# Kernel tuning notes

Measured on AMD Instinct MI355X. Metric: run time of the kernel, lower is better.

Reference implementation:

```python
import jax, jax.numpy as jnp
import numpy as np

# Grid / modeling constants (match init_kwargs)
NX, NY = 512, 512
NT = 400
ORDER = 8
NE = ORDER // 2          # halo width
H = 10.0                 # grid spacing (m)
DT = 0.001               # time step (s)
DIMX = NX + ORDER
DIMY = NY + ORDER
# 8th-order second-derivative FD coefficients
C0, C1, C2, C3, C4 = -205.0 / 72.0, 8.0 / 5.0, -1.0 / 5.0, 8.0 / 315.0, -1.0 / 560.0
_COEF = (C1, C2, C3, C4)


def setup_inputs() -> dict:
    key = jax.random.key(0)
    k1, k2 = jax.random.split(key)
    # realistic acoustic velocity model, 1500-2500 m/s
    vel = 1500.0 + 1000.0 * jax.random.uniform(k1, (NX, NY), dtype=jnp.float32)
    w = jax.random.normal(k2, (NT,), dtype=jnp.float32)  # source wavelet
    return {"vel": vel, "w": w, "sx": 256, "sy": 4, "ry": 4}


def _laplacian(u):
    # order-8 cross stencil in x and y (grid is (dimy, dimx), x fast)
    l = 2.0 * C0 * u
    for k, c in zip((1, 2, 3, 4), _COEF):
        l = l + c * (jnp.roll(u, k, 0) + jnp.roll(u, -k, 0)
                     + jnp.roll(u, k, 1) + jnp.roll(u, -k, 1))
    return l


def _forward(vel, w, sx, sy, ry):
    # vel: (nx, ny) y-fast -> vpad: (dimy, dimx) x-fast, replication padded
    vpad = jnp.pad(vel.T, NE, mode="edge")
    scale = (vpad * DT) ** 2 / (H * H)          # (v*dt/h)^2 per cell
    mask = jnp.zeros((DIMY, DIMX), vel.dtype).at[NE:NE + NY, NE:NE + NX].set(1.0)
    iy, ix = sy + NE, sx + NE
    src_amp = (vpad[iy, ix] * DT) ** 2           # dt^2 * v^2 at source

    def step(carry, wt):
        u1, u2 = carry
        lap = _laplacian(u2)
        u3 = (2.0 * u2 - u1 + scale * lap) * mask  # zero Dirichlet halo
        u3 = u3.at[iy, ix].add(wt * src_amp)       # source injection
        rec = u3[ry + NE, NE:NE + NX]              # record x-line at depth ry
        return (u2, u3), rec

    u0 = jnp.zeros((DIMY, DIMX), vel.dtype)
    _, frd = jax.lax.scan(jax.checkpoint(step), (u0, u0), w)
    return frd  # (nt, nx)


def reference(vel, w, sx, sy, ry):
    return _forward(vel, w, sx, sy, ry)
```

## Files before the change

### kernel.cpp

```cpp
#include <hip/hip_runtime.h>

typedef float f32x4 __attribute__((ext_vector_type(4)));

#define NXg   512
#define NYg   512
#define NTt   400
#define DIMg  520
#define DTc   0.001f
#define Hc    10.0f

#define TILE   80
#define TSTR   84
#define NQROW  20
#define NQUADS (TILE*NQROW)

#define C0f (-205.0f/72.0f)
#define C1f (8.0f/5.0f)
#define C2f (-1.0f/5.0f)
#define C3f (8.0f/315.0f)
#define C4f (-1.0f/560.0f)

__global__ void time2d_init(const float* __restrict__ vel,
                            const float* __restrict__ w,
                            const int* __restrict__ sxp,
                            const int* __restrict__ syp,
                            const int* __restrict__ ryp,
                            float* __restrict__ scale,
                            float* __restrict__ fields,
                            float* __restrict__ params) {
    int idx = blockIdx.x * blockDim.x + threadIdx.x;
    if (idx < DIMg * DIMg) {
        int y = idx / DIMg;
        int x = idx - y * DIMg;
        float s = 0.0f;
        if (y >= 4 && y < 516 && x >= 4 && x < 516) {
            float v = vel[(x - 4) * NYg + (y - 4)] * DTc;
            s = v * v / (Hc * Hc);
        }
        scale[idx] = s;
    }
    for (int i = idx; i < 4 * DIMg * DIMg; i += gridDim.x * blockDim.x)
        fields[i] = 0.0f;
    if (idx < NTt) {
        const int sx = *sxp, sy = *syp;
        const float va = vel[sx * NYg + sy] * DTc;
        params[4 + idx] = w[idx] * (va * va);
    }
    if (idx == 0) {
        int* pi = (int*)params;
        pi[0] = *syp + 4;
        pi[1] = *sxp + 4;
        pi[2] = *ryp + 4;
    }
}

template<int K>
__launch_bounds__(512)
__global__ void time2d_chunk(const float* __restrict__ Ps,
                             const float* __restrict__ Cs,
                             float* __restrict__ Pd,
                             float* __restrict__ Cd,
                             const float* __restrict__ scale,
                             const float* __restrict__ params,
                             float* __restrict__ out,
                             int t0)
{
    const int tid = threadIdx.x;
    const int bx = blockIdx.x, by = blockIdx.y;
    const int lx0 = bx * 32 - 20, ly0 = by * 32 - 20;

    const int* pi = (const int*)params;
    const int srcY = pi[0], srcX = pi[1], recY = pi[2];

    __shared__ float lds[2][TILE * TSTR];

    #pragma unroll
    for (int ii = 0; ii < 4; ++ii) {
        const int pos = tid + 512 * ii;
        if (pos < NQUADS) {
            const int ty = pos / NQROW, txq = pos - ty * NQROW;
            const int gy = ly0 + ty, gx = lx0 + txq * 4;
            f32x4 v = (f32x4)0.0f;
            if ((unsigned)gy < 520u && (unsigned)gx < 517u)
                v = *(const f32x4*)&Cs[gy * DIMg + gx];
            *(f32x4*)&lds[0][ty * TSTR + txq * 4] = v;
        }
    }

    const int ct = tid;
    const bool active = (ct < 360);
    const int xc = ct % NQROW, yg = ct / NQROW;
    const int x4 = xc * 4;
    const int rb = 4 + yg * 4;
    const int gx0 = lx0 + x4;
    const bool ownedCol = (xc >= 6 && xc < 14);
    const bool ownedRow = ((unsigned)(rb - 24) < 32u);

    f32x4 scq[4], prevq[4], valq[4];
    int srcI = -1, srcJ = 0;
    bool rec[4];
    #pragma unroll
    for (int i = 0; i < 4; ++i) {
        const int gy = ly0 + rb + i;
        f32x4 s = (f32x4)0.0f, pv = (f32x4)0.0f;
        if (active && (unsigned)gy < 520u && (unsigned)gx0 < 517u) {
            s  = *(const f32x4*)&scale[gy * DIMg + gx0];
            pv = *(const f32x4*)&Ps[gy * DIMg + gx0];
        }
        scq[i] = s; prevq[i] = pv;
        #pragma unroll
        for (int j = 0; j < 4; ++j)
            if (gy == srcY && gx0 + j == srcX) { srcI = i; srcJ = j; }
        rec[i] = active && ownedCol && ownedRow && (gy == recY);
    }

    float injs[K];
    #pragma unroll
    for (int k = 0; k < K; ++k)
        injs[k] = (srcI >= 0) ? params[4 + t0 + k] : 0.0f;

    __syncthreads();

    int p = 0;
    #pragma unroll
    for (int k = 0; k < K; ++k) {
        const float* cur = lds[p];
        float* nxt = lds[p ^ 1];
        if (active) {
            f32x4 win[12];
            #pragma unroll
            for (int m = 0; m < 12; ++m)
                win[m] = *(const f32x4*)&cur[(rb - 4 + m) * TSTR + x4];
            #pragma unroll
            for (int i = 0; i < 4; ++i) {
                const int y = rb + i;
                const f32x4 lq = *(const f32x4*)&cur[y * TSTR + x4 - 4];
                const f32x4 rq = *(const f32x4*)&cur[y * TSTR + x4 + 4];
                float h[12];
                #pragma unroll
                for (int j = 0; j < 4; ++j) {
                    h[j] = lq[j]; h[4 + j] = win[4 + i][j]; h[8 + j] = rq[j];
                }
                f32x4 nv;
                #pragma unroll
                for (int j = 0; j < 4; ++j) {
                    const float ctr = h[4 + j];
                    const float lap = 2.0f * C0f * ctr
                      + C1f * (win[3 + i][j] + win[5 + i][j] + h[3 + j] + h[5 + j])
                      + C2f * (win[2 + i][j] + win[6 + i][j] + h[2 + j] + h[6 + j])
                      + C3f * (win[1 + i][j] + win[7 + i][j] + h[1 + j] + h[7 + j])
                      + C4f * (win[0 + i][j] + win[8 + i][j] + h[0 + j] + h[8 + j]);
                    float nvj = 2.0f * ctr - prevq[i][j] + scq[i][j] * lap;
                    if (srcI == i && srcJ == j) nvj += injs[k];
                    nv[j] = nvj;
                    prevq[i][j] = ctr;
                }
                *(f32x4*)&nxt[y * TSTR + x4] = nv;
                valq[i] = nv;
                if (rec[i])
                    *(f32x4*)&out[(size_t)(t0 + k) * NXg + (gx0 - 4)] = nv;
            }
        }
        __syncthreads();
        p ^= 1;
    }

    if (active && ownedCol && ownedRow) {
        #pragma unroll
        for (int i = 0; i < 4; ++i) {
            const size_t g = (size_t)(ly0 + rb + i) * DIMg + gx0;
            *(f32x4*)&Pd[g] = prevq[i];
            *(f32x4*)&Cd[g] = valq[i];
        }
    }
}

extern "C" void kernel_launch(void* const* d_in, const int* in_sizes, int n_in,
                              void* d_out, int out_size, void* d_ws, size_t ws_size,
                              hipStream_t stream) {
    const float* vel = (const float*)d_in[0];
    const float* w   = (const float*)d_in[1];
    const int*   sx  = (const int*)d_in[2];
    const int*   sy  = (const int*)d_in[3];
    const int*   ry  = (const int*)d_in[4];
    float* out = (float*)d_out;

    float* ws     = (float*)d_ws;
    float* scale  = ws;
    float* params = ws + DIMg * DIMg;
    float* fld    = params + 512;
    float* P[2]   = { fld,               fld + 2 * DIMg * DIMg };
    float* C[2]   = { fld + DIMg * DIMg, fld + 3 * DIMg * DIMg };

    time2d_init<<<(DIMg * DIMg + 255) / 256, 256, 0, stream>>>(
        vel, w, sx, sy, ry, scale, fld, params);

    dim3 grid(16, 16);
    for (int c = 0; c < 66; ++c) {
        const int s = c & 1, d = s ^ 1;
        time2d_chunk<6><<<grid, 512, 0, stream>>>(P[s], C[s], P[d], C[d],
                                                  scale, params, out, c * 6);
    }
    {
        const int c = 66, s = c & 1, d = s ^ 1;
        time2d_chunk<4><<<grid, 512, 0, stream>>>(P[s], C[s], P[d], C[d],
                                                  scale, params, out, 396);
    }
}
```

Before: 880.9 us.

## Shrink temporal-blocking tiles to 64x48 with 4 steps per launch

Temporal blocking changes from 6 steps per launch on 80x80 tiles (16x16 grid) to 4 steps per launch on 64x48 tiles (16x32 grid). Each thread now computes 2 rows instead of 4, all 320 threads are active, and the final barrier is skipped. The aim is to raise occupancy and block count (512 blocks, launch bounds of 320 with a minimum of 3) and to cut idle threads and redundant halo work. In exchange there are more launches (100 vs 67) and a larger halo-to-interior ratio per step, so more global traffic per output.

After: 871.8 us. No clear change (-1.0%).

```diff
diff --git a/kernel.cpp b/kernel.cpp
--- a/kernel.cpp
+++ b/kernel.cpp
@@ -8,11 +8,14 @@
 #define DIMg  520
 #define DTc   0.001f
 #define Hc    10.0f
-
-#define TILE   80
-#define TSTR   84
-#define NQROW  20
-#define NQUADS (TILE*NQROW)
+#define KSTEP 4
+#define NCHUNK 100
+
+#define TILE_W 64
+#define TILE_H 48
+#define TSTR   68
+#define NQROW  16
+#define NQUADS (TILE_H * NQROW)
 
 #define C0f (-205.0f/72.0f)
 #define C1f (8.0f/5.0f)
@@ -55,7 +58,7 @@
 }
 
 template<int K>
-__launch_bounds__(512)
+__launch_bounds__(320, 3)
 __global__ void time2d_chunk(const float* __restrict__ Ps,
                              const float* __restrict__ Cs,
                              float* __restrict__ Pd,
@@ -67,18 +70,18 @@
 {
     const int tid = threadIdx.x;
     const int bx = blockIdx.x, by = blockIdx.y;
-    const int lx0 = bx * 32 - 20, ly0 = by * 32 - 20;
+    const int lx0 = bx * 32 - 12, ly0 = by * 16 - 12;
 
     const int* pi = (const int*)params;
     const int srcY = pi[0], srcX = pi[1], recY = pi[2];
 
-    __shared__ float lds[2][TILE * TSTR];
-
-    #pragma unroll
-    for (int ii = 0; ii < 4; ++ii) {
-        const int pos = tid + 512 * ii;
+    __shared__ float lds[2][TILE_H * TSTR];
+
+    #pragma unroll
+    for (int ii = 0; ii < 3; ++ii) {
+        const int pos = tid + 320 * ii;
         if (pos < NQUADS) {
-            const int ty = pos / NQROW, txq = pos - ty * NQROW;
+            const int ty = pos >> 4, txq = pos & 15;
             const int gy = ly0 + ty, gx = lx0 + txq * 4;
             f32x4 v = (f32x4)0.0f;
             if ((unsigned)gy < 520u && (unsigned)gx < 517u)
@@ -87,23 +90,22 @@
         }
     }
 
-    const int ct = tid;
-    const bool active = (ct < 360);
-    const int xc = ct % NQROW, yg = ct / NQROW;
+    const int xc = tid & 15, pr = tid >> 4;
     const int x4 = xc * 4;
-    const int rb = 4 + yg * 4;
+    const int rb = 4 + pr * 2;
     const int gx0 = lx0 + x4;
-    const bool ownedCol = (xc >= 6 && xc < 14);
-    const bool ownedRow = ((unsigned)(rb - 24) < 32u);
-
-    f32x4 scq[4], prevq[4], valq[4];
+    const bool ownedCol = (xc >= 4 && xc < 12);
+
+    f32x4 scq[2], prevq[2], valq[2];
     int srcI = -1, srcJ = 0;
-    bool rec[4];
-    #pragma unroll
-    for (int i = 0; i < 4; ++i) {
+    bool rec[2], ownRow[2];
+    int gyv[2];
+    #pragma unroll
+    for (int i = 0; i < 2; ++i) {
         const int gy = ly0 + rb + i;
+        gyv[i] = gy;
         f32x4 s = (f32x4)0.0f, pv = (f32x4)0.0f;
-        if (active && (unsigned)gy < 520u && (unsigned)gx0 < 517u) {
+        if ((unsigned)gy < 520u && (unsigned)gx0 < 517u) {
             s  = *(const f32x4*)&scale[gy * DIMg + gx0];
             pv = *(const f32x4*)&Ps[gy * DIMg + gx0];
         }
@@ -111,7 +113,8 @@
         #pragma unroll
         for (int j = 0; j < 4; ++j)
             if (gy == srcY && gx0 + j == srcX) { srcI = i; srcJ = j; }
-        rec[i] = active && ownedCol && ownedRow && (gy == recY);
+        ownRow[i] = ((unsigned)(rb + i - 16) < 16u);
+        rec[i] = ownedCol && ownRow[i] && (gy == recY);
     }
 
     float injs[K];
@@ -126,51 +129,51 @@
     for (int k = 0; k < K; ++k) {
         const float* cur = lds[p];
         float* nxt = lds[p ^ 1];
-        if (active) {
-            f32x4 win[12];
+        f32x4 win[10];
+        #pragma unroll
+        for (int m = 0; m < 10; ++m)
+            win[m] = *(const f32x4*)&cur[(rb - 4 + m) * TSTR + x4];
+        #pragma unroll
+        for (int i = 0; i < 2; ++i) {
+            const int y = rb + i;
+            const f32x4 lq = *(const f32x4*)&cur[y * TSTR + x4 - 4];
+            const f32x4 rq = *(const f32x4*)&cur[y * TSTR + x4 + 4];
+            float h[12];
             #pragma unroll
-            for (int m = 0; m < 12; ++m)
-                win[m] = *(const f32x4*)&cur[(rb - 4 + m) * TSTR + x4];
+            for (int j = 0; j < 4; ++j) {
+                h[j] = lq[j]; h[4 + j] = win[4 + i][j]; h[8 + j] = rq[j];
+            }
+            f32x4 nv;
             #pragma unroll
-            for (int i = 0; i < 4; ++i) {
-                const int y = rb + i;
-                const f32x4 lq = *(const f32x4*)&cur[y * TSTR + x4 - 4];
-                const f32x4 rq = *(const f32x4*)&cur[y * TSTR + x4 + 4];
-                float h[12];
-                #pragma unroll
-                for (int j = 0; j < 4; ++j) {
-                    h[j] = lq[j]; h[4 + j] = win[4 + i][j]; h[8 + j] = rq[j];
-                }
-                f32x4 nv;
-                #pragma unroll
-                for (int j = 0; j < 4; ++j) {
-                    const float ctr = h[4 + j];
-                    const float lap = 2.0f * C0f * ctr
-                      + C1f * (win[3 + i][j] + win[5 + i][j] + h[3 + j] + h[5 + j])
-                      + C2f * (win[2 + i][j] + win[6 + i][j] + h[2 + j] + h[6 + j])
-                      + C3f * (win[1 + i][j] + win[7 + i][j] + h[1 + j] + h[7 + j])
-                      + C4f * (win[0 + i][j] + win[8 + i][j] + h[0 + j] + h[8 + j]);
-                    float nvj = 2.0f * ctr - prevq[i][j] + scq[i][j] * lap;
-                    if (srcI == i && srcJ == j) nvj += injs[k];
-                    nv[j] = nvj;
-                    prevq[i][j] = ctr;
-                }
-                *(f32x4*)&nxt[y * TSTR + x4] = nv;
-                valq[i] = nv;
-                if (rec[i])
-                    *(f32x4*)&out[(size_t)(t0 + k) * NXg + (gx0 - 4)] = nv;
+            for (int j = 0; j < 4; ++j) {
+                const float ctr = h[4 + j];
+                const float lap = 2.0f * C0f * ctr
+                  + C1f * (win[3 + i][j] + win[5 + i][j] + h[3 + j] + h[5 + j])
+                  + C2f * (win[2 + i][j] + win[6 + i][j] + h[2 + j] + h[6 + j])
+                  + C3f * (win[1 + i][j] + win[7 + i][j] + h[1 + j] + h[7 + j])
+                  + C4f * (win[0 + i][j] + win[8 + i][j] + h[0 + j] + h[8 + j]);
+                float nvj = 2.0f * ctr - prevq[i][j] + scq[i][j] * lap;
+                if (srcI == i && srcJ == j) nvj += injs[k];
+                nv[j] = nvj;
+                prevq[i][j] = ctr;
             }
-        }
-        __syncthreads();
+            *(f32x4*)&nxt[y * TSTR + x4] = nv;
+            valq[i] = nv;
+            if (rec[i])
+                *(f32x4*)&out[(size_t)(t0 + k) * NXg + (gx0 - 4)] = nv;
+        }
+        if (k < K - 1) __syncthreads();
         p ^= 1;
     }
 
-    if (active && ownedCol && ownedRow) {
-        #pragma unroll
-        for (int i = 0; i < 4; ++i) {
-            const size_t g = (size_t)(ly0 + rb + i) * DIMg + gx0;
-            *(f32x4*)&Pd[g] = prevq[i];
-            *(f32x4*)&Cd[g] = valq[i];
+    if (ownedCol) {
+        #pragma unroll
+        for (int i = 0; i < 2; ++i) {
+            if (ownRow[i]) {
+                const size_t g = (size_t)gyv[i] * DIMg + gx0;
+                *(f32x4*)&Pd[g] = prevq[i];
+                *(f32x4*)&Cd[g] = valq[i];
+            }
         }
     }
 }
@@ -195,15 +198,11 @@
     time2d_init<<<(DIMg * DIMg + 255) / 256, 256, 0, stream>>>(
         vel, w, sx, sy, ry, scale, fld, params);
 
-    dim3 grid(16, 16);
-    for (int c = 0; c < 66; ++c) {
+    dim3 grid(16, 32);
+    for (int c = 0; c < NCHUNK; ++c) {
         const int s = c & 1, d = s ^ 1;
-        time2d_chunk<6><<<grid, 512, 0, stream>>>(P[s], C[s], P[d], C[d],
-                                                  scale, params, out, c * 6);
-    }
-    {
-        const int c = 66, s = c & 1, d = s ^ 1;
-        time2d_chunk<4><<<grid, 512, 0, stream>>>(P[s], C[s], P[d], C[d],
-                                                  scale, params, out, 396);
+        time2d_chunk<KSTEP><<<grid, 320, 0, stream>>>(P[s], C[s], P[d], C[d],
+                                                      scale, params, out,
+                                                      c * KSTEP);
     }
 }
```

## Use 32x16 owned tiles with shrinking trapezoid compute and buffered receiver writes

Applied to the files above, without the earlier changes.

The temporal-blocking tile changes from a 32x32 owned region in an 80x80 halo tile to 32x16 owned in an 80x64 tile. The grid doubles to 512 blocks of 320 threads with launch bounds asking for two blocks per CU. Each time step now computes only the shrinking valid trapezoid instead of the full halo region. Receiver outputs are buffered in registers and written after the loop, and the last barrier is dropped. This improves occupancy and skips redundant halo work, at the cost of a higher halo-to-owned ratio in y and more global reads per owned cell.

Measured after the change: 1.329 ms. +50.8%, slower.

```diff
diff --git a/kernel.cpp b/kernel.cpp
--- a/kernel.cpp
+++ b/kernel.cpp
@@ -6,13 +6,15 @@
 #define NYg   512
 #define NTt   400
 #define DIMg  520
+#define NCELL (DIMg*DIMg)
 #define DTc   0.001f
 #define Hc    10.0f
 
-#define TILE   80
+#define TILE_W 80
+#define TILE_H 64
 #define TSTR   84
 #define NQROW  20
-#define NQUADS (TILE*NQROW)
+#define NQUADS (TILE_H * NQROW)
 
 #define C0f (-205.0f/72.0f)
 #define C1f (8.0f/5.0f)
@@ -29,7 +31,7 @@
                             float* __restrict__ fields,
                             float* __restrict__ params) {
     int idx = blockIdx.x * blockDim.x + threadIdx.x;
-    if (idx < DIMg * DIMg) {
+    if (idx < NCELL) {
         int y = idx / DIMg;
         int x = idx - y * DIMg;
         float s = 0.0f;
@@ -39,7 +41,7 @@
         }
         scale[idx] = s;
     }
-    for (int i = idx; i < 4 * DIMg * DIMg; i += gridDim.x * blockDim.x)
+    for (int i = idx; i < 4 * NCELL; i += gridDim.x * blockDim.x)
         fields[i] = 0.0f;
     if (idx < NTt) {
         const int sx = *sxp, sy = *syp;
@@ -55,7 +57,7 @@
 }
 
 template<int K>
-__launch_bounds__(512)
+__launch_bounds__(320, 2)
 __global__ void time2d_chunk(const float* __restrict__ Ps,
                              const float* __restrict__ Cs,
                              float* __restrict__ Pd,
@@ -67,41 +69,39 @@
 {
     const int tid = threadIdx.x;
     const int bx = blockIdx.x, by = blockIdx.y;
-    const int lx0 = bx * 32 - 20, ly0 = by * 32 - 20;
+    const int lx0 = bx * 32 - 20, ly0 = by * 16 - 20;
 
     const int* pi = (const int*)params;
     const int srcY = pi[0], srcX = pi[1], recY = pi[2];
 
-    __shared__ float lds[2][TILE * TSTR];
+    __shared__ float lds[2][TILE_H * TSTR];
 
     #pragma unroll
     for (int ii = 0; ii < 4; ++ii) {
-        const int pos = tid + 512 * ii;
-        if (pos < NQUADS) {
-            const int ty = pos / NQROW, txq = pos - ty * NQROW;
-            const int gy = ly0 + ty, gx = lx0 + txq * 4;
-            f32x4 v = (f32x4)0.0f;
-            if ((unsigned)gy < 520u && (unsigned)gx < 517u)
-                v = *(const f32x4*)&Cs[gy * DIMg + gx];
-            *(f32x4*)&lds[0][ty * TSTR + txq * 4] = v;
-        }
-    }
-
-    const int ct = tid;
-    const bool active = (ct < 360);
-    const int xc = ct % NQROW, yg = ct / NQROW;
+        const int pos = tid + 320 * ii;
+        const int ty = pos / NQROW, txq = pos - ty * NQROW;
+        const int gy = ly0 + ty, gx = lx0 + txq * 4;
+        f32x4 v = (f32x4)0.0f;
+        if ((unsigned)gy < 520u && (unsigned)gx < 517u)
+            v = *(const f32x4*)&Cs[gy * DIMg + gx];
+        *(f32x4*)&lds[0][ty * TSTR + txq * 4] = v;
+    }
+
+    const int xc = tid % NQROW, pr = tid / NQROW;
+    const bool active = (pr < 14);
     const int x4 = xc * 4;
-    const int rb = 4 + yg * 4;
+    const int rb = 4 + pr * 4;
     const int gx0 = lx0 + x4;
     const bool ownedCol = (xc >= 6 && xc < 14);
-    const bool ownedRow = ((unsigned)(rb - 24) < 32u);
-
-    f32x4 scq[4], prevq[4], valq[4];
+
+    f32x4 scq[4], prevq[4], valq[4], recv[K];
     int srcI = -1, srcJ = 0;
     bool rec[4];
+    int gyv[4];
     #pragma unroll
     for (int i = 0; i < 4; ++i) {
         const int gy = ly0 + rb + i;
+        gyv[i] = gy;
         f32x4 s = (f32x4)0.0f, pv = (f32x4)0.0f;
         if (active && (unsigned)gy < 520u && (unsigned)gx0 < 517u) {
             s  = *(const f32x4*)&scale[gy * DIMg + gx0];
@@ -111,7 +111,8 @@
         #pragma unroll
         for (int j = 0; j < 4; ++j)
             if (gy == srcY && gx0 + j == srcX) { srcI = i; srcJ = j; }
-        rec[i] = active && ownedCol && ownedRow && (gy == recY);
+        const bool ownRow = ((unsigned)(rb + i - 24) < 16u);
+        rec[i] = ownedCol && ownRow && (gy == recY);
     }
 
     float injs[K];
@@ -126,7 +127,10 @@
     for (int k = 0; k < K; ++k) {
         const float* cur = lds[p];
         float* nxt = lds[p ^ 1];
-        if (active) {
+        const bool docomp = active
+            && (rb >= 4 * k + 4) && (rb <= 56 - 4 * k)
+            && (xc >= k + 1) && (xc <= 18 - k);
+        if (docomp) {
             f32x4 win[12];
             #pragma unroll
             for (int m = 0; m < 12; ++m)
@@ -157,20 +161,27 @@
                 }
                 *(f32x4*)&nxt[y * TSTR + x4] = nv;
                 valq[i] = nv;
-                if (rec[i])
-                    *(f32x4*)&out[(size_t)(t0 + k) * NXg + (gx0 - 4)] = nv;
+                if (rec[i]) recv[k] = nv;
             }
         }
-        __syncthreads();
+        if (k < K - 1) __syncthreads();
         p ^= 1;
     }
 
-    if (active && ownedCol && ownedRow) {
+    if (rec[0] | rec[1] | rec[2] | rec[3]) {
+        #pragma unroll
+        for (int k = 0; k < K; ++k)
+            *(f32x4*)&out[(size_t)(t0 + k) * NXg + (gx0 - 4)] = recv[k];
+    }
+
+    if (ownedCol) {
         #pragma unroll
         for (int i = 0; i < 4; ++i) {
-            const size_t g = (size_t)(ly0 + rb + i) * DIMg + gx0;
-            *(f32x4*)&Pd[g] = prevq[i];
-            *(f32x4*)&Cd[g] = valq[i];
+            if ((unsigned)(rb + i - 24) < 16u) {
+                const size_t g = (size_t)gyv[i] * DIMg + gx0;
+                *(f32x4*)&Pd[g] = prevq[i];
+                *(f32x4*)&Cd[g] = valq[i];
+            }
         }
     }
 }
@@ -187,23 +198,23 @@
 
     float* ws     = (float*)d_ws;
     float* scale  = ws;
-    float* params = ws + DIMg * DIMg;
+    float* params = ws + NCELL;
     float* fld    = params + 512;
-    float* P[2]   = { fld,               fld + 2 * DIMg * DIMg };
-    float* C[2]   = { fld + DIMg * DIMg, fld + 3 * DIMg * DIMg };
-
-    time2d_init<<<(DIMg * DIMg + 255) / 256, 256, 0, stream>>>(
+    float* P[2]   = { fld,           fld + 2 * NCELL };
+    float* C[2]   = { fld + NCELL,   fld + 3 * NCELL };
+
+    time2d_init<<<(NCELL + 255) / 256, 256, 0, stream>>>(
         vel, w, sx, sy, ry, scale, fld, params);
 
-    dim3 grid(16, 16);
+    dim3 grid(16, 32);
     for (int c = 0; c < 66; ++c) {
         const int s = c & 1, d = s ^ 1;
-        time2d_chunk<6><<<grid, 512, 0, stream>>>(P[s], C[s], P[d], C[d],
+        time2d_chunk<6><<<grid, 320, 0, stream>>>(P[s], C[s], P[d], C[d],
                                                   scale, params, out, c * 6);
     }
     {
-        const int c = 66, s = c & 1, d = s ^ 1;
-        time2d_chunk<4><<<grid, 512, 0, stream>>>(P[s], C[s], P[d], C[d],
+        const int s = 66 & 1, d = s ^ 1;
+        time2d_chunk<4><<<grid, 320, 0, stream>>>(P[s], C[s], P[d], C[d],
                                                   scale, params, out, 396);
     }
 }
```
